# Kernel optimization log

Hardware: AMD Instinct MI355X
Metric: run time of the kernel (lower is better)

Reference implementation:

```python
import jax, jax.numpy as jnp
import numpy as np

MAX_Z = 54  # atomic numbers up to iodine (53)
_mv = np.full(MAX_Z, 4.0, np.float32)
for z, v in {6: 4, 7: 3, 8: 2, 16: 6, 9: 1, 17: 1, 35: 1, 53: 1, 15: 5, 1: 1}.items():
    _mv[z] = v
_vdw = np.full(MAX_Z, 1.6, np.float32)  # default_radius = 1.6
for z, r in {1: 1.2, 6: 1.7, 7: 1.55, 8: 1.52, 9: 1.47, 15: 1.8, 16: 1.8, 17: 1.75, 35: 1.85, 53: 1.98}.items():
    _vdw[z] = r
_bl = np.full((MAX_Z, MAX_Z), 1.5, np.float32)  # default_length = 1.5
for (a, b), L in {(6, 6): 1.54, (6, 7): 1.47, (6, 8): 1.43, (6, 16): 1.82, (6, 9): 1.35, (6, 17): 1.77, (6, 1): 1.09, (7, 7): 1.45, (7, 8): 1.40, (7, 1): 1.01, (8, 8): 1.48, (8, 1): 0.96, (16, 16): 2.05, (15, 8): 1.63}.items():
    _bl[a, b] = L
    _bl[b, a] = L  # symmetric == tuple(sorted(...)) lookup
MAX_VAL = jnp.asarray(_mv)
VDW = jnp.asarray(_vdw)
BOND = jnp.asarray(_bl)
BIG = 1e9  # stands in for torch's float('inf') diagonal mask


def _forward(pos, edge_index, atom_types):
    N = pos.shape[0]
    row, col = edge_index[0], edge_index[1]
    # --- valence violations: scatter-add out-degree per atom ---
    bond_counts = jnp.zeros((N,), pos.dtype).at[row].add(1.0)
    violation = jnp.maximum(bond_counts - MAX_VAL[atom_types], 0.0)  # >0 iff counts > max_val
    loss = jnp.sum(violation ** 2)
    # Sequential valence push. Original loops atoms in ascending order and each atom's
    # neighbors in edge-list order; a stable sort of edges by row reproduces exactly that
    # visitation order, so a scan over sorted edges matches the sequential semantics
    # (pos_new[i] updates feed later direction computations).
    order = jnp.argsort(row)  # jnp.argsort is stable
    rs, cs = row[order], col[order]

    def step(p, rc):
        r, c = rc
        v = violation[r]
        d = p[r] - p[c]
        dist = jnp.linalg.norm(d) + 1e-8
        return p.at[r].add(jnp.where(v > 0, d / dist * v * 1e-3, 0.0)), None

    pos_new, _ = jax.lax.scan(step, pos, (rs, cs))
    # --- bond-length correction (gather per edge, scatter back per atom) ---
    bond_vec = pos_new[row] - pos_new[col]                        # [E,3]
    cur_len = jnp.linalg.norm(bond_vec, axis=-1, keepdims=True)   # [E,1]
    tgt_len = BOND[atom_types[row], atom_types[col]][:, None]     # [E,1]
    loss = loss + jnp.mean(jnp.abs(cur_len - tgt_len) ** 2)
    ratio = jnp.clip(tgt_len / (cur_len + 1e-8), 0.98, 1.02)
    adj = (bond_vec * ratio - bond_vec) * 0.01
    pos_new = pos_new + jnp.zeros_like(pos).at[row].add(adj * 0.5).at[col].add(-adj * 0.5)
    # --- steric clash repulsion over all atom pairs (cdist) ---
    sq = jnp.sum(pos_new ** 2, axis=-1)
    d2 = sq[:, None] + sq[None, :] - 2.0 * (pos_new @ pos_new.T)  # [N,N]
    eye = jnp.eye(N, dtype=bool)
    dist = jnp.sqrt(jnp.maximum(jnp.where(eye, 1.0, d2), 1e-20))
    dist = jnp.where(eye, BIG, dist)  # diagonal masked to +inf in the original
    rad = VDW[atom_types]
    min_d = (rad[:, None] + rad[None, :]) * 0.8
    loss = loss + jnp.sum(jax.nn.relu(min_d - dist) ** 2) / 2.0
    # original loops unordered clash pairs i<j updating i and j symmetrically; the full
    # symmetric double sum below is mathematically identical and avoids an [N,N,3] tensor:
    mask = (dist < min_d) & (dist > 1e-8)
    coeff = jnp.where(mask, (min_d - dist) * 0.005 * 0.5 / dist, 0.0)  # [N,N]
    steric = coeff.sum(axis=1)[:, None] * pos_new - coeff @ pos_new    # sum_j c_ij (p_i - p_j)
    return pos_new + steric, loss * 0.1


def setup_inputs() -> dict:
    key = jax.random.key(0)
    k1, k2, k3, k4 = jax.random.split(key, 4)
    N, E = 8192, 32768
    pos = jax.random.normal(k1, (N, 3), jnp.float32) * 6.0  # coords in an ~Angstrom-scale blob
    elements = jnp.array([1, 6, 7, 8, 9, 15, 16, 17], jnp.int32)  # H C N O F P S Cl
    atom_types = elements[jax.random.randint(k2, (N,), 0, 8)]
    edge_index = jnp.stack([jax.random.randint(k3, (E,), 0, N),
                            jax.random.randint(k4, (E,), 0, N)]).astype(jnp.int32)
    return {"pos": pos, "edge_index": edge_index, "atom_types": atom_types}


def reference(pos, edge_index, atom_types):
    return _forward(pos, edge_index, atom_types)
```

## Files before the change

### kernel.cpp

```cpp
#include <hip/hip_runtime.h>
#include <math.h>

#define NA 8192
#define NE 32768
#define NT 256
#define NIB 16

#define WS_DEG      0
#define WS_LOSS     (WS_DEG + NA)
#define WS_DD       (WS_LOSS + 4)
#define WS_ZERO_END (WS_DD + 3*NA)
#define WS_PART     ((WS_ZERO_END + 3) & ~3)

__device__ __forceinline__ float maxval_of(int z) {
    switch (z) {
        case 1: return 1.f; case 6: return 4.f; case 7: return 3.f; case 8: return 2.f;
        case 9: return 1.f; case 15: return 5.f; case 16: return 6.f; case 17: return 1.f;
        case 35: return 1.f; case 53: return 1.f; default: return 4.f;
    }
}
__device__ __forceinline__ float vdw_of(int z) {
    switch (z) {
        case 1: return 1.2f; case 6: return 1.7f; case 7: return 1.55f; case 8: return 1.52f;
        case 9: return 1.47f; case 15: return 1.8f; case 16: return 1.8f; case 17: return 1.75f;
        case 35: return 1.85f; case 53: return 1.98f; default: return 1.6f;
    }
}
__device__ __forceinline__ float bond_of(int a, int b) {
    int lo = a < b ? a : b, hi = a < b ? b : a;
    switch (lo * 64 + hi) {
        case 6*64+6:   return 1.54f;
        case 6*64+7:   return 1.47f;
        case 6*64+8:   return 1.43f;
        case 6*64+16:  return 1.82f;
        case 6*64+9:   return 1.35f;
        case 6*64+17:  return 1.77f;
        case 1*64+6:   return 1.09f;
        case 7*64+7:   return 1.45f;
        case 7*64+8:   return 1.40f;
        case 1*64+7:   return 1.01f;
        case 8*64+8:   return 1.48f;
        case 1*64+8:   return 0.96f;
        case 16*64+16: return 2.05f;
        case 8*64+15:  return 1.63f;
        default:       return 1.5f;
    }
}
__device__ __forceinline__ float viol_of(int d, int z) {
    return fmaxf((float)d - maxval_of(z), 0.f);
}

__device__ __forceinline__ float wave_reduce_sum(float x) {
    #pragma unroll
    for (int off = 32; off > 0; off >>= 1) x += __shfl_down(x, off);
    return x;
}

__global__ void k_degbond(const int* __restrict__ row, const int* __restrict__ col,
                          const int* __restrict__ types, const float* __restrict__ pos,
                          int* __restrict__ deg, float* __restrict__ dD,
                          float* __restrict__ lossAcc) {
    int e = blockIdx.x * NT + threadIdx.x;
    float l1 = 0.f;
    if (e < NE) {
        int r = row[e], c = col[e];
        atomicAdd(&deg[r], 1);
        float bx = pos[3*r]   - pos[3*c];
        float by = pos[3*r+1] - pos[3*c+1];
        float bz = pos[3*r+2] - pos[3*c+2];
        float cur = sqrtf(bx*bx + by*by + bz*bz);
        float tgt = bond_of(types[r], types[c]);
        float diff = cur - tgt;
        l1 = diff * diff;
        float ratio = tgt / (cur + 1e-8f);
        ratio = fminf(fmaxf(ratio, 0.98f), 1.02f);
        float s = (ratio - 1.f) * 0.01f * 0.5f;
        atomicAdd(&dD[3*r],   bx * s);
        atomicAdd(&dD[3*r+1], by * s);
        atomicAdd(&dD[3*r+2], bz * s);
        atomicAdd(&dD[3*c],   -bx * s);
        atomicAdd(&dD[3*c+1], -by * s);
        atomicAdd(&dD[3*c+2], -bz * s);
    }
    float p1 = wave_reduce_sum(l1);
    if ((threadIdx.x & 63) == 0 && p1 != 0.f) atomicAdd(&lossAcc[1], p1);
}

__global__ void k_push(const int* __restrict__ row, const int* __restrict__ col,
                       const int* __restrict__ types, const int* __restrict__ deg,
                       const float* __restrict__ pos, float* __restrict__ dD,
                       float* __restrict__ lossAcc) {
    int e = blockIdx.x * NT + threadIdx.x;
    if (e < NE) {
        int r = row[e];
        float v = viol_of(deg[r], types[r]);
        int c = col[e];
        if (v > 0.f && c != r) {
            float dx = pos[3*r]   - pos[3*c];
            float dy = pos[3*r+1] - pos[3*c+1];
            float dz = pos[3*r+2] - pos[3*c+2];
            float dist = sqrtf(dx*dx + dy*dy + dz*dz) + 1e-8f;
            float sc = v * 1e-3f / dist;
            atomicAdd(&dD[3*r],   dx * sc);
            atomicAdd(&dD[3*r+1], dy * sc);
            atomicAdd(&dD[3*r+2], dz * sc);
        }
    }
    float l0 = 0.f;
    if (e < NA) {
        float v = viol_of(deg[e], types[e]);
        l0 = v * v;
    }
    float p0 = wave_reduce_sum(l0);
    if ((threadIdx.x & 63) == 0 && p0 != 0.f) atomicAdd(&lossAcc[0], p0);
}

__device__ __forceinline__ void steric_pair(const float4 p, const float4 q,
                                            float& cs, float& sx, float& sy, float& sz,
                                            float& ll) {
    float dx = p.x - q.x, dy = p.y - q.y, dz = p.z - q.z;
    float d2 = fmaf(dx, dx, fmaf(dy, dy, dz * dz));
    float md = p.w + q.w;
    float rinv = rsqrtf(fmaxf(d2, 1e-12f));
    float dist = d2 * rinv;
    float t1 = md - dist;
    bool ok = (t1 > 0.f) && (d2 > 1e-12f);
    float t1c = ok ? t1 : 0.f;
    ll = fmaf(t1c, t1c, ll);
    float co = t1c * rinv;
    cs += co;
    sx = fmaf(co, q.x, sx);
    sy = fmaf(co, q.y, sy);
    sz = fmaf(co, q.z, sz);
}

__global__ void __launch_bounds__(NT)
k_steric(const float* __restrict__ pos, const float* __restrict__ dD,
         const int* __restrict__ types, float4* __restrict__ partial,
         float* __restrict__ lossAcc, int jchunk) {
    __shared__ float4 sm[256];
    const int t = threadIdx.x;
    const int yb = blockIdx.x >> 4;
    const int ib = blockIdx.x & 15;
    if (t < jchunk) {
        int j = yb * jchunk + t;
        sm[t] = make_float4(pos[3*j]   + dD[3*j],
                            pos[3*j+1] + dD[3*j+1],
                            pos[3*j+2] + dD[3*j+2],
                            vdw_of(types[j]) * 0.8f);
    }
    const int i0 = ib * 512 + t;
    const int i1 = i0 + 256;
    float4 p0 = make_float4(pos[3*i0] + dD[3*i0], pos[3*i0+1] + dD[3*i0+1],
                            pos[3*i0+2] + dD[3*i0+2], vdw_of(types[i0]) * 0.8f);
    float4 p1 = make_float4(pos[3*i1] + dD[3*i1], pos[3*i1+1] + dD[3*i1+1],
                            pos[3*i1+2] + dD[3*i1+2], vdw_of(types[i1]) * 0.8f);
    __syncthreads();
    float cs0 = 0.f, sx0 = 0.f, sy0 = 0.f, sz0 = 0.f;
    float cs1 = 0.f, sx1 = 0.f, sy1 = 0.f, sz1 = 0.f;
    float ll = 0.f;
    #pragma unroll 8
    for (int jj = 0; jj < jchunk; jj++) {
        float4 q = sm[jj];
        steric_pair(p0, q, cs0, sx0, sy0, sz0, ll);
        steric_pair(p1, q, cs1, sx1, sy1, sz1, ll);
    }
    partial[yb * NA + i0] = make_float4(cs0, sx0, sy0, sz0);
    partial[yb * NA + i1] = make_float4(cs1, sx1, sy1, sz1);
    float part = wave_reduce_sum(ll);
    if ((t & 63) == 0 && part != 0.f) atomicAdd(&lossAcc[2], part);
}

__global__ void k_reduce(const float* __restrict__ pos, const float* __restrict__ dD,
                         const float4* __restrict__ partial,
                         const float* __restrict__ lossAcc, float* __restrict__ out,
                         int jsplit) {
    int a = blockIdx.x * NT + threadIdx.x;
    float cs = 0.f, sx = 0.f, sy = 0.f, sz = 0.f;
    #pragma unroll 8
    for (int y = 0; y < jsplit; y++) {
        float4 u = partial[y * NA + a];
        cs += u.x; sx += u.y; sy += u.z; sz += u.w;
    }
    float px = pos[3*a]   + dD[3*a];
    float py = pos[3*a+1] + dD[3*a+1];
    float pz = pos[3*a+2] + dD[3*a+2];
    float c = 1.f + cs * 0.0025f;
    out[3*a]   = px * c - sx * 0.0025f;
    out[3*a+1] = py * c - sy * 0.0025f;
    out[3*a+2] = pz * c - sz * 0.0025f;
    if (a == 0) {
        float loss = lossAcc[0] + lossAcc[1] * (1.f / NE) + lossAcc[2] * 0.5f;
        out[3*NA] = loss * 0.1f;
    }
}

extern "C" void kernel_launch(void* const* d_in, const int* in_sizes, int n_in,
                              void* d_out, int out_size, void* d_ws, size_t ws_size,
                              hipStream_t stream) {
    (void)in_sizes; (void)n_in; (void)out_size;
    const float* pos   = (const float*)d_in[0];
    const int*   eidx  = (const int*)d_in[1];
    const int*   types = (const int*)d_in[2];
    const int* row = eidx;
    const int* col = eidx + NE;

    int*   ws_i = (int*)d_ws;
    float* ws_f = (float*)d_ws;
    int*    deg     = ws_i + WS_DEG;
    float*  lossAcc = ws_f + WS_LOSS;
    float*  dD      = ws_f + WS_DD;
    float4* partial = (float4*)(ws_f + WS_PART);
    float*  out     = (float*)d_out;

    size_t need64 = ((size_t)WS_PART + (size_t)4 * 64 * NA) * 4;
    int jsplit = (ws_size >= need64) ? 64 : 32;
    int jchunk = NA / jsplit;

    hipMemsetAsync(d_ws, 0, (size_t)WS_ZERO_END * 4, stream);
    k_degbond<<<NE/NT, NT, 0, stream>>>(row, col, types, pos, deg, dD, lossAcc);
    k_push   <<<NE/NT, NT, 0, stream>>>(row, col, types, deg, pos, dD, lossAcc);
    k_steric <<<jsplit*NIB, NT, 0, stream>>>(pos, dD, types, partial, lossAcc, jchunk);
    k_reduce <<<NA/NT, NT, 0, stream>>>(pos, dD, partial, lossAcc, out, jsplit);
}
```

Baseline: 154.2 us.

## Fuse bond-length and valence-push edge passes and fix steric j-split at 32

Degree counting moves into its own small kernel. The bond-length correction and the valence push are then merged into one edge kernel that gathers positions once and issues a single set of atomic adds on the row atom, carrying both contributions. The steric split over j is now fixed at compile time to 32 chunks of 256, instead of picking 64 when the workspace allows. That halves the number of partial buffers that k_reduce has to sum, but launches fewer steric blocks, which may leave some compute units underused.

```diff
diff --git a/kernel.cpp b/kernel.cpp
--- a/kernel.cpp
+++ b/kernel.cpp
@@ -4,6 +4,8 @@
 #define NA 8192
 #define NE 32768
 #define NT 256
+#define JSPLIT 32
+#define JCHUNK (NA / JSPLIT)
 #define NIB 16
 
 #define WS_DEG      0
@@ -56,15 +58,19 @@
     return x;
 }
 
-__global__ void k_degbond(const int* __restrict__ row, const int* __restrict__ col,
-                          const int* __restrict__ types, const float* __restrict__ pos,
-                          int* __restrict__ deg, float* __restrict__ dD,
-                          float* __restrict__ lossAcc) {
+__global__ void k_deg(const int* __restrict__ row, int* __restrict__ deg) {
     int e = blockIdx.x * NT + threadIdx.x;
-    float l1 = 0.f;
+    if (e < NE) atomicAdd(&deg[row[e]], 1);
+}
+
+__global__ void k_edge(const int* __restrict__ row, const int* __restrict__ col,
+                       const int* __restrict__ types, const int* __restrict__ deg,
+                       const float* __restrict__ pos, float* __restrict__ dD,
+                       float* __restrict__ lossAcc) {
+    int e = blockIdx.x * NT + threadIdx.x;
+    float l1 = 0.f, l0 = 0.f;
     if (e < NE) {
         int r = row[e], c = col[e];
-        atomicAdd(&deg[r], 1);
         float bx = pos[3*r]   - pos[3*c];
         float by = pos[3*r+1] - pos[3*c+1];
         float bz = pos[3*r+2] - pos[3*c+2];
@@ -75,44 +81,26 @@
         float ratio = tgt / (cur + 1e-8f);
         ratio = fminf(fmaxf(ratio, 0.98f), 1.02f);
         float s = (ratio - 1.f) * 0.01f * 0.5f;
-        atomicAdd(&dD[3*r],   bx * s);
-        atomicAdd(&dD[3*r+1], by * s);
-        atomicAdd(&dD[3*r+2], bz * s);
+        float v = viol_of(deg[r], types[r]);
+        float sc = (v > 0.f) ? (v * 1e-3f / (cur + 1e-8f)) : 0.f;
+        float rs = s + sc;
+        atomicAdd(&dD[3*r],   bx * rs);
+        atomicAdd(&dD[3*r+1], by * rs);
+        atomicAdd(&dD[3*r+2], bz * rs);
         atomicAdd(&dD[3*c],   -bx * s);
         atomicAdd(&dD[3*c+1], -by * s);
         atomicAdd(&dD[3*c+2], -bz * s);
     }
-    float p1 = wave_reduce_sum(l1);
-    if ((threadIdx.x & 63) == 0 && p1 != 0.f) atomicAdd(&lossAcc[1], p1);
-}
-
-__global__ void k_push(const int* __restrict__ row, const int* __restrict__ col,
-                       const int* __restrict__ types, const int* __restrict__ deg,
-                       const float* __restrict__ pos, float* __restrict__ dD,
-                       float* __restrict__ lossAcc) {
-    int e = blockIdx.x * NT + threadIdx.x;
-    if (e < NE) {
-        int r = row[e];
-        float v = viol_of(deg[r], types[r]);
-        int c = col[e];
-        if (v > 0.f && c != r) {
-            float dx = pos[3*r]   - pos[3*c];
-            float dy = pos[3*r+1] - pos[3*c+1];
-            float dz = pos[3*r+2] - pos[3*c+2];
-            float dist = sqrtf(dx*dx + dy*dy + dz*dz) + 1e-8f;
-            float sc = v * 1e-3f / dist;
-            atomicAdd(&dD[3*r],   dx * sc);
-            atomicAdd(&dD[3*r+1], dy * sc);
-            atomicAdd(&dD[3*r+2], dz * sc);
-        }
-    }
-    float l0 = 0.f;
     if (e < NA) {
         float v = viol_of(deg[e], types[e]);
         l0 = v * v;
     }
+    float p1 = wave_reduce_sum(l1);
     float p0 = wave_reduce_sum(l0);
-    if ((threadIdx.x & 63) == 0 && p0 != 0.f) atomicAdd(&lossAcc[0], p0);
+    if ((threadIdx.x & 63) == 0) {
+        if (p1 != 0.f) atomicAdd(&lossAcc[1], p1);
+        if (p0 != 0.f) atomicAdd(&lossAcc[0], p0);
+    }
 }
 
 __device__ __forceinline__ void steric_pair(const float4 p, const float4 q,
@@ -137,18 +125,17 @@
 __global__ void __launch_bounds__(NT)
 k_steric(const float* __restrict__ pos, const float* __restrict__ dD,
          const int* __restrict__ types, float4* __restrict__ partial,
-         float* __restrict__ lossAcc, int jchunk) {
-    __shared__ float4 sm[256];
+         float* __restrict__ lossAcc) {
+    __shared__ float4 sm[JCHUNK];
     const int t = threadIdx.x;
-    const int yb = blockIdx.x >> 4;
-    const int ib = blockIdx.x & 15;
-    if (t < jchunk) {
-        int j = yb * jchunk + t;
-        sm[t] = make_float4(pos[3*j]   + dD[3*j],
-                            pos[3*j+1] + dD[3*j+1],
-                            pos[3*j+2] + dD[3*j+2],
-                            vdw_of(types[j]) * 0.8f);
-    }
+    const int b = blockIdx.x;
+    const int yb = b >> 4;
+    const int ib = b & 15;
+    int j = yb * JCHUNK + t;
+    sm[t] = make_float4(pos[3*j]   + dD[3*j],
+                        pos[3*j+1] + dD[3*j+1],
+                        pos[3*j+2] + dD[3*j+2],
+                        vdw_of(types[j]) * 0.8f);
     const int i0 = ib * 512 + t;
     const int i1 = i0 + 256;
     float4 p0 = make_float4(pos[3*i0] + dD[3*i0], pos[3*i0+1] + dD[3*i0+1],
@@ -160,7 +147,7 @@
     float cs1 = 0.f, sx1 = 0.f, sy1 = 0.f, sz1 = 0.f;
     float ll = 0.f;
     #pragma unroll 8
-    for (int jj = 0; jj < jchunk; jj++) {
+    for (int jj = 0; jj < JCHUNK; jj++) {
         float4 q = sm[jj];
         steric_pair(p0, q, cs0, sx0, sy0, sz0, ll);
         steric_pair(p1, q, cs1, sx1, sy1, sz1, ll);
@@ -173,12 +160,11 @@
 
 __global__ void k_reduce(const float* __restrict__ pos, const float* __restrict__ dD,
                          const float4* __restrict__ partial,
-                         const float* __restrict__ lossAcc, float* __restrict__ out,
-                         int jsplit) {
+                         const float* __restrict__ lossAcc, float* __restrict__ out) {
     int a = blockIdx.x * NT + threadIdx.x;
     float cs = 0.f, sx = 0.f, sy = 0.f, sz = 0.f;
     #pragma unroll 8
-    for (int y = 0; y < jsplit; y++) {
+    for (int y = 0; y < JSPLIT; y++) {
         float4 u = partial[y * NA + a];
         cs += u.x; sx += u.y; sy += u.z; sz += u.w;
     }
@@ -198,7 +184,7 @@
 extern "C" void kernel_launch(void* const* d_in, const int* in_sizes, int n_in,
                               void* d_out, int out_size, void* d_ws, size_t ws_size,
                               hipStream_t stream) {
-    (void)in_sizes; (void)n_in; (void)out_size;
+    (void)in_sizes; (void)n_in; (void)out_size; (void)ws_size;
     const float* pos   = (const float*)d_in[0];
     const int*   eidx  = (const int*)d_in[1];
     const int*   types = (const int*)d_in[2];
@@ -213,13 +199,9 @@
     float4* partial = (float4*)(ws_f + WS_PART);
     float*  out     = (float*)d_out;
 
-    size_t need64 = ((size_t)WS_PART + (size_t)4 * 64 * NA) * 4;
-    int jsplit = (ws_size >= need64) ? 64 : 32;
-    int jchunk = NA / jsplit;
-
     hipMemsetAsync(d_ws, 0, (size_t)WS_ZERO_END * 4, stream);
-    k_degbond<<<NE/NT, NT, 0, stream>>>(row, col, types, pos, deg, dD, lossAcc);
-    k_push   <<<NE/NT, NT, 0, stream>>>(row, col, types, deg, pos, dD, lossAcc);
-    k_steric <<<jsplit*NIB, NT, 0, stream>>>(pos, dD, types, partial, lossAcc, jchunk);
-    k_reduce <<<NA/NT, NT, 0, stream>>>(pos, dD, partial, lossAcc, out, jsplit);
-}
+    k_deg   <<<NE/NT, NT, 0, stream>>>(row, deg);
+    k_edge  <<<NE/NT, NT, 0, stream>>>(row, col, types, deg, pos, dD, lossAcc);
+    k_steric<<<JSPLIT*NIB, NT, 0, stream>>>(pos, dD, types, partial, lossAcc);
+    k_reduce<<<NA/NT, NT, 0, stream>>>(pos, dD, partial, lossAcc, out);
+}
```

Measured after the change: 130.1 us. -15.6%, faster.
